# Optimization experiments

Measured on AMD Instinct MI355X. Metric: run time of the kernel, lower is better.

Reference implementation:

```python
import jax, jax.numpy as jnp
import numpy as np

N_SUP, D = 4096, 128
N_CLASSES, SHOTS = 128, 32          # balanced episode: N_SUP = N_CLASSES * SHOTS
N_QUERY = 65536
N_BOOT = 8                          # num_bootstrap_samples


def setup_inputs() -> dict:
    key = jax.random.key(0)
    k_sup, k_q, k_boot = jax.random.split(key, 3)
    support_set_repr = jax.random.normal(k_sup, (N_SUP, D), dtype=jnp.float32)
    # balanced, sorted labels: class c owns contiguous block [c*SHOTS, (c+1)*SHOTS)
    support_labels = (jnp.arange(N_SUP, dtype=jnp.int32) // SHOTS).astype(jnp.int32)
    query_set_repr = jax.random.normal(k_q, (N_QUERY, D), dtype=jnp.float32)
    # externalized torch.randint(0, num_samples, (B, num_samples)) per class
    bootstrap_indices = jax.random.randint(
        k_boot, (N_BOOT, N_CLASSES, SHOTS), 0, SHOTS, dtype=jnp.int32)
    return {
        "support_set_repr": support_set_repr,
        "support_labels": support_labels,
        "query_set_repr": query_set_repr,
        "bootstrap_indices": bootstrap_indices,
    }


def reference(support_set_repr, support_labels, query_set_repr, bootstrap_indices):
    B, C, S = bootstrap_indices.shape
    d = support_set_repr.shape[-1]
    # labels are sorted & balanced (arange // SHOTS), so per-class gather == reshape
    class_repr = support_set_repr.reshape(C, S, d)              # [C, S, D]
    # fused bootstrap gather: [B, C, S, D]
    boot = jnp.take_along_axis(class_repr[None], bootstrap_indices[..., None], axis=2)
    protos = boot.mean(axis=2)                                   # [B, C, D]
    # cdist(q, protos, p=2) via ||q||^2 + ||p||^2 - 2 q.p
    q2 = jnp.sum(query_set_repr * query_set_repr, axis=-1)       # [NQ]
    p2 = jnp.sum(protos * protos, axis=-1)                       # [B, C]
    qp = jnp.einsum('qd,bcd->bqc', query_set_repr, protos)       # [B, NQ, C]
    d2 = q2[None, :, None] + p2[:, None, :] - 2.0 * qp
    dists = jnp.sqrt(jnp.maximum(d2, 0.0))                       # [B, NQ, C]
    # logits = mean over bootstraps of -dists
    return -dists.mean(axis=0)                                   # [NQ, C]
```

## Files before the change

### kernel.cpp

```cpp
#include <hip/hip_runtime.h>
#include <hip/hip_bf16.h>


#define DIM   128
#define NCLS  128
#define SHOTS 32
#define NB    8
#define NQ    65536

using short8 = __attribute__((ext_vector_type(8))) short;
using f32x4  = __attribute__((ext_vector_type(4))) float;

__device__ __forceinline__ unsigned short f2bf(float x) {
  union { float f; unsigned u; } v; v.f = x;
  unsigned r = v.u + 0x7fffu + ((v.u >> 16) & 1u);
  return (unsigned short)(r >> 16);
}

__device__ __forceinline__ short8 pack8_bf16(float4 a, float4 b) {
  __hip_bfloat162 p0 = __float22bfloat162_rn(make_float2(a.x, a.y));
  __hip_bfloat162 p1 = __float22bfloat162_rn(make_float2(a.z, a.w));
  __hip_bfloat162 p2 = __float22bfloat162_rn(make_float2(b.x, b.y));
  __hip_bfloat162 p3 = __float22bfloat162_rn(make_float2(b.z, b.w));
  union { __hip_bfloat162 h[4]; short8 s; } u;
  u.h[0] = p0; u.h[1] = p1; u.h[2] = p2; u.h[3] = p3;
  return u.s;
}

__device__ __forceinline__ float fast_sqrt(float x) {
#if __has_builtin(__builtin_amdgcn_sqrtf)
  return __builtin_amdgcn_sqrtf(x);
#else
  return sqrtf(x);
#endif
}

__global__ __launch_bounds__(128) void proto_kernel(
    const float* __restrict__ sup, const int* __restrict__ bidx,
    unsigned short* __restrict__ pfrag, float* __restrict__ p2) {
  int bc = blockIdx.x;
  int c  = bc & (NCLS - 1);
  int d  = threadIdx.x;
  __shared__ int   sidx[SHOTS];
  __shared__ float wsum[2];
  if (d < SHOTS) sidx[d] = bidx[bc * SHOTS + d];
  __syncthreads();
  float acc = 0.f;
  const float* base = sup + c * SHOTS * DIM + d;
  #pragma unroll
  for (int s = 0; s < SHOTS; ++s) acc += base[sidx[s] * DIM];
  float proto = acc * (1.0f / 32.0f);

  int b     = bc >> 7;
  int ct    = c >> 4, l15c = c & 15;
  int kiter = d >> 5, quad = (d >> 3) & 3, j = d & 7;
  int lane  = l15c + (quad << 4);
  int slot  = (b * 8 + ct) * 4 + kiter;
  pfrag[slot * 512 + lane * 8 + j] = f2bf(proto * -0.03125f);

  float sq = proto * proto;
  #pragma unroll
  for (int off = 32; off > 0; off >>= 1) sq += __shfl_down(sq, off, 64);
  if ((d & 63) == 0) wsum[d >> 6] = sq;
  __syncthreads();
  if (d == 0) p2[bc] = (wsum[0] + wsum[1]) * (1.0f / 64.0f);
}

#define SLOT_STRIDE 520

__global__ __launch_bounds__(256) void dist_kernel(
    const float* __restrict__ q, const uint4* __restrict__ pfrag,
    const float* __restrict__ p2, float* __restrict__ out) {
  int tid  = threadIdx.x;
  int w    = tid >> 6, lane = tid & 63;
  int l15  = lane & 15, quad = lane >> 4;
  int q0   = blockIdx.x << 5;

  __shared__ unsigned short aflds[8 * SLOT_STRIDE];
  __shared__ float q2s[32];

  {
    int rloc  = w * 8 + (lane >> 3);
    int chunk = lane & 7;
    const float* src = q + (size_t)(q0 + rloc) * DIM + chunk * 16;
    float4 x0 = *reinterpret_cast<const float4*>(src);
    float4 x1 = *reinterpret_cast<const float4*>(src + 4);
    float4 x2 = *reinterpret_cast<const float4*>(src + 8);
    float4 x3 = *reinterpret_cast<const float4*>(src + 12);
    float s = x0.x*x0.x + x0.y*x0.y + x0.z*x0.z + x0.w*x0.w
            + x1.x*x1.x + x1.y*x1.y + x1.z*x1.z + x1.w*x1.w
            + x2.x*x2.x + x2.y*x2.y + x2.z*x2.z + x2.w*x2.w
            + x3.x*x3.x + x3.y*x3.y + x3.z*x3.z + x3.w*x3.w;
    s += __shfl_down(s, 4, 8);
    s += __shfl_down(s, 2, 8);
    s += __shfl_down(s, 1, 8);
    if (chunk == 0) q2s[rloc] = s;

    int mt = rloc >> 4, m = rloc & 15, i = chunk >> 1, h = chunk & 1;
    unsigned short* base = &aflds[(mt * 4 + i) * SLOT_STRIDE];
    *reinterpret_cast<short8*>(&base[((h * 2 + 0) * 16 + m) * 8]) = pack8_bf16(x0, x1);
    *reinterpret_cast<short8*>(&base[((h * 2 + 1) * 16 + m) * 8]) = pack8_bf16(x2, x3);
  }
  __syncthreads();

  short8 af[2][4];
  #pragma unroll
  for (int mt = 0; mt < 2; ++mt)
    #pragma unroll
    for (int k = 0; k < 4; ++k)
      af[mt][k] = *reinterpret_cast<const short8*>(
          &aflds[(mt * 4 + k) * SLOT_STRIDE + lane * 8]);

  f32x4 q2r[2];
  #pragma unroll
  for (int mt = 0; mt < 2; ++mt)
    #pragma unroll
    for (int r = 0; r < 4; ++r)
      q2r[mt][r] = q2s[mt * 16 + quad * 4 + r] * (1.0f / 64.0f);

  float p2v[NB][2];
  #pragma unroll
  for (int b = 0; b < NB; ++b)
    #pragma unroll
    for (int jj = 0; jj < 2; ++jj)
      p2v[b][jj] = p2[b * NCLS + (w * 2 + jj) * 16 + l15];

  f32x4 oacc[2][2];
  #pragma unroll
  for (int i = 0; i < 2; ++i)
    #pragma unroll
    for (int jj = 0; jj < 2; ++jj)
      oacc[i][jj] = (f32x4){0.f, 0.f, 0.f, 0.f};

  uint4 bufX[8], bufY[8];

  #define LOAD_B(BUF, B)                                                      \
    {                                                                         \
      _Pragma("unroll")                                                       \
      for (int jj = 0; jj < 2; ++jj) {                                        \
        int ct = w * 2 + jj;                                                  \
        const uint4* bp = pfrag + (size_t)(((B) * 8 + ct) * 4) * 64 + lane;   \
        _Pragma("unroll")                                                     \
        for (int k = 0; k < 4; ++k) BUF[jj * 4 + k] = bp[k * 64];             \
      }                                                                       \
    }

  #define COMPUTE_B(BUF, B)                                                   \
    {                                                                         \
      _Pragma("unroll")                                                       \
      for (int jj = 0; jj < 2; ++jj) {                                        \
        f32x4 qp0, qp1;                                                       \
        _Pragma("unroll")                                                     \
        for (int r = 0; r < 4; ++r) {                                         \
          qp0[r] = q2r[0][r] + p2v[B][jj];                                    \
          qp1[r] = q2r[1][r] + p2v[B][jj];                                    \
        }                                                                     \
        _Pragma("unroll")                                                     \
        for (int k = 0; k < 4; ++k) {                                         \
          short8 bfk = __builtin_bit_cast(short8, BUF[jj * 4 + k]);           \
          qp0 = __builtin_amdgcn_mfma_f32_16x16x32_bf16(af[0][k], bfk, qp0, 0, 0, 0); \
          qp1 = __builtin_amdgcn_mfma_f32_16x16x32_bf16(af[1][k], bfk, qp1, 0, 0, 0); \
        }                                                                     \
        _Pragma("unroll")                                                     \
        for (int r = 0; r < 4; ++r) {                                         \
          oacc[0][jj][r] += fast_sqrt(fmaxf(qp0[r], 0.0f));                   \
          oacc[1][jj][r] += fast_sqrt(fmaxf(qp1[r], 0.0f));                   \
        }                                                                     \
      }                                                                       \
    }

  LOAD_B(bufX, 0)
  #pragma unroll 1
  for (int i = 0; i < NB; i += 2) {
    LOAD_B(bufY, i + 1)
    COMPUTE_B(bufX, i)
    LOAD_B(bufX, (i + 2) & (NB - 1))
    COMPUTE_B(bufY, i + 1)
  }
  #undef LOAD_B
  #undef COMPUTE_B

  #pragma unroll
  for (int mt2 = 0; mt2 < 2; ++mt2)
    #pragma unroll
    for (int jj = 0; jj < 2; ++jj) {
      int col = (w * 2 + jj) * 16 + l15;
      #pragma unroll
      for (int r = 0; r < 4; ++r) {
        int row = q0 + mt2 * 16 + quad * 4 + r;
        out[(size_t)row * NCLS + col] = -oacc[mt2][jj][r];
      }
    }
}

extern "C" void kernel_launch(void* const* d_in, const int* in_sizes, int n_in,
                              void* d_out, int out_size, void* d_ws, size_t ws_size,
                              hipStream_t stream) {
  const float* sup   = (const float*)d_in[0];
  const float* query = (const float*)d_in[2];
  const int*   bidx  = (const int*)d_in[3];
  float* out = (float*)d_out;

  unsigned short* pfrag = (unsigned short*)d_ws;
  float* p2 = (float*)((char*)d_ws + (size_t)NB * NCLS * DIM * 2);

  proto_kernel<<<NB * NCLS, 128, 0, stream>>>(sup, bidx, pfrag, p2);
  dist_kernel<<<NQ / 32, 256, 0, stream>>>(query, (const uint4*)pfrag, p2, out);
}
```

Before: 113.3 us.

## Double query rows per block to reuse prototype fragments across four M-tiles

Each dist_kernel block now handles 64 queries instead of 32, loading query rows in two passes and running four MFMA M-tiles per prototype B-fragment. This halves the global/L2 traffic for prototype fragments per query and halves the grid size. The cost is more registers (af, qp, oacc doubled), with launch_bounds(256,2) added to cap occupancy pressure, and fewer blocks to fill the GPU.

```diff
diff --git a/kernel.cpp b/kernel.cpp
--- a/kernel.cpp
+++ b/kernel.cpp
@@ -68,19 +68,20 @@
 
 #define SLOT_STRIDE 520
 
-__global__ __launch_bounds__(256) void dist_kernel(
+__global__ __launch_bounds__(256, 2) void dist_kernel(
     const float* __restrict__ q, const uint4* __restrict__ pfrag,
     const float* __restrict__ p2, float* __restrict__ out) {
   int tid  = threadIdx.x;
   int w    = tid >> 6, lane = tid & 63;
   int l15  = lane & 15, quad = lane >> 4;
-  int q0   = blockIdx.x << 5;
-
-  __shared__ unsigned short aflds[8 * SLOT_STRIDE];
-  __shared__ float q2s[32];
-
-  {
-    int rloc  = w * 8 + (lane >> 3);
+  int q0   = blockIdx.x << 6;
+
+  __shared__ unsigned short aflds[16 * SLOT_STRIDE];
+  __shared__ float q2s[64];
+
+  #pragma unroll
+  for (int pass = 0; pass < 2; ++pass) {
+    int rloc  = w * 16 + pass * 8 + (lane >> 3);
     int chunk = lane & 7;
     const float* src = q + (size_t)(q0 + rloc) * DIM + chunk * 16;
     float4 x0 = *reinterpret_cast<const float4*>(src);
@@ -103,17 +104,17 @@
   }
   __syncthreads();
 
-  short8 af[2][4];
-  #pragma unroll
-  for (int mt = 0; mt < 2; ++mt)
+  short8 af[4][4];
+  #pragma unroll
+  for (int mt = 0; mt < 4; ++mt)
     #pragma unroll
     for (int k = 0; k < 4; ++k)
       af[mt][k] = *reinterpret_cast<const short8*>(
           &aflds[(mt * 4 + k) * SLOT_STRIDE + lane * 8]);
 
-  f32x4 q2r[2];
-  #pragma unroll
-  for (int mt = 0; mt < 2; ++mt)
+  f32x4 q2r[4];
+  #pragma unroll
+  for (int mt = 0; mt < 4; ++mt)
     #pragma unroll
     for (int r = 0; r < 4; ++r)
       q2r[mt][r] = q2s[mt * 16 + quad * 4 + r] * (1.0f / 64.0f);
@@ -125,12 +126,12 @@
     for (int jj = 0; jj < 2; ++jj)
       p2v[b][jj] = p2[b * NCLS + (w * 2 + jj) * 16 + l15];
 
-  f32x4 oacc[2][2];
-  #pragma unroll
-  for (int i = 0; i < 2; ++i)
+  f32x4 oacc[4][2];
+  #pragma unroll
+  for (int mt = 0; mt < 4; ++mt)
     #pragma unroll
     for (int jj = 0; jj < 2; ++jj)
-      oacc[i][jj] = (f32x4){0.f, 0.f, 0.f, 0.f};
+      oacc[mt][jj] = (f32x4){0.f, 0.f, 0.f, 0.f};
 
   uint4 bufX[8], bufY[8];
 
@@ -149,23 +150,24 @@
     {                                                                         \
       _Pragma("unroll")                                                       \
       for (int jj = 0; jj < 2; ++jj) {                                        \
-        f32x4 qp0, qp1;                                                       \
-        _Pragma("unroll")                                                     \
-        for (int r = 0; r < 4; ++r) {                                         \
-          qp0[r] = q2r[0][r] + p2v[B][jj];                                    \
-          qp1[r] = q2r[1][r] + p2v[B][jj];                                    \
-        }                                                                     \
+        f32x4 qp[4];                                                          \
+        _Pragma("unroll")                                                     \
+        for (int mt = 0; mt < 4; ++mt)                                        \
+          _Pragma("unroll")                                                   \
+          for (int r = 0; r < 4; ++r)                                         \
+            qp[mt][r] = q2r[mt][r] + p2v[B][jj];                              \
         _Pragma("unroll")                                                     \
         for (int k = 0; k < 4; ++k) {                                         \
           short8 bfk = __builtin_bit_cast(short8, BUF[jj * 4 + k]);           \
-          qp0 = __builtin_amdgcn_mfma_f32_16x16x32_bf16(af[0][k], bfk, qp0, 0, 0, 0); \
-          qp1 = __builtin_amdgcn_mfma_f32_16x16x32_bf16(af[1][k], bfk, qp1, 0, 0, 0); \
+          _Pragma("unroll")                                                   \
+          for (int mt = 0; mt < 4; ++mt)                                      \
+            qp[mt] = __builtin_amdgcn_mfma_f32_16x16x32_bf16(af[mt][k], bfk, qp[mt], 0, 0, 0); \
         }                                                                     \
         _Pragma("unroll")                                                     \
-        for (int r = 0; r < 4; ++r) {                                         \
-          oacc[0][jj][r] += fast_sqrt(fmaxf(qp0[r], 0.0f));                   \
-          oacc[1][jj][r] += fast_sqrt(fmaxf(qp1[r], 0.0f));                   \
-        }                                                                     \
+        for (int mt = 0; mt < 4; ++mt)                                        \
+          _Pragma("unroll")                                                   \
+          for (int r = 0; r < 4; ++r)                                         \
+            oacc[mt][jj][r] += fast_sqrt(fmaxf(qp[mt][r], 0.0f));             \
       }                                                                       \
     }
 
@@ -181,7 +183,7 @@
   #undef COMPUTE_B
 
   #pragma unroll
-  for (int mt2 = 0; mt2 < 2; ++mt2)
+  for (int mt2 = 0; mt2 < 4; ++mt2)
     #pragma unroll
     for (int jj = 0; jj < 2; ++jj) {
       int col = (w * 2 + jj) * 16 + l15;
@@ -205,5 +207,5 @@
   float* p2 = (float*)((char*)d_ws + (size_t)NB * NCLS * DIM * 2);
 
   proto_kernel<<<NB * NCLS, 128, 0, stream>>>(sup, bidx, pfrag, p2);
-  dist_kernel<<<NQ / 32, 256, 0, stream>>>(query, (const uint4*)pfrag, p2, out);
-}
+  dist_kernel<<<NQ / 64, 256, 0, stream>>>(query, (const uint4*)pfrag, p2, out);
+}
```

After: 110.8 us. 1.02x faster.
